# Performance work log

Measured on AMD Instinct MI355X. Metric: run time of the kernel, lower is better.

The kernel has to match this reference:

```python
import jax, jax.numpy as jnp
import numpy as np

B, H, F, Z, T = 8192, 256, 128, 64, 43
STEPS = T - 3


def setup_inputs() -> dict:
    key = jax.random.key(0)
    ks = jax.random.split(key, 24)
    def nrm(k, shape, s=0.05):
        return (jax.random.normal(k, shape) * s).astype(jnp.float32)
    inp = {}
    inp["h_i"] = nrm(ks[0], (B, H), 1.0)                      # encoder context state
    t = jax.random.uniform(ks[1], (B, T)) * T                  # event timestamps, sorted
    inp["input_t"] = jnp.sort(t, axis=1).astype(jnp.float32)
    inp["eps_inf"] = jax.random.normal(ks[2], (STEPS, B, Z), dtype=jnp.float32)
    inp["eps_prior"] = jax.random.normal(ks[3], (STEPS, B, Z), dtype=jnp.float32)
    in_dim = Z + H + F
    inp["Wx"] = nrm(ks[4], (in_dim, 4 * H))
    inp["Wh"] = nrm(ks[5], (H, 4 * H))
    inp["b_lstm"] = jnp.zeros((4 * H,), jnp.float32)
    dims = [(H, F), (F, F), (F, F), (2 * H + 2 * F, Z), (Z, Z), (Z, Z), (2 * H + F, Z), (Z, Z), (Z, Z)]
    for i, (di, do) in enumerate(dims, 1):
        inp[f"w{i}"] = nrm(ks[5 + i], (di, do))
        inp[f"b{i}"] = jnp.zeros((do,), jnp.float32)
    inp["alpha"] = (jax.random.uniform(ks[20], (1, 1)) * 0.1).astype(jnp.float32)
    inp["beta"] = (jax.random.uniform(ks[21], (1, 1)) * 0.1).astype(jnp.float32)
    inp["mu0"] = (jax.random.uniform(ks[22], (1, 1)) * 0.1).astype(jnp.float32)
    return inp


def _forward(h_i, input_t, eps_inf, eps_prior, Wx, Wh, b_lstm,
             w1, b1, w2, b2, w3, b3, w4, b4, w5, b5, w6, b6, w7, b7, w8, b8, w9, b9,
             alpha, beta, mu0):
    batch = h_i.shape[0]
    idxs = jnp.arange(T)

    def dense(x, w, b):
        return jax.nn.relu(x @ w + b)

    def step(carry, xs):
        h, c, z_j, y_prev = carry
        e_i, e_p, j = xs
        # LSTM cell (Keras gate order i, f, c, o)
        x = jnp.concatenate([z_j, h_i, y_prev], axis=1)
        gates = x @ Wx + h @ Wh + b_lstm
        i_g, f_g, g_g, o_g = jnp.split(gates, 4, axis=1)
        c_new = jax.nn.sigmoid(f_g) * c + jax.nn.sigmoid(i_g) * jnp.tanh(g_g)
        h_new = jax.nn.sigmoid(o_g) * jnp.tanh(c_new)
        # Hawkes intensity over events strictly before current_time_index = j+3
        t_idx = j + 3
        t_cur = jnp.take(input_t, t_idx, axis=1)[:, None]          # [B,1]
        mask = idxs < t_idx                                         # [T]
        diff = jnp.where(mask[None, :], input_t - t_cur, -jnp.inf)
        trig = jnp.sum(jnp.exp(diff), axis=1, keepdims=True) * beta[0, 0]
        intensity = mu0[0, 0] + alpha[0, 0] * trig                  # [B,1]
        # original code gates state[1] (the cell state slot) with the intensity
        c_gated = intensity * c_new
        y = dense(dense(dense(h_new, w1, b1), w2, b2), w3, b3)
        # inference network (s_j = ungated c_new, mirroring the TF code)
        inf_in = jnp.concatenate([h_i, c_new, y, y_prev], axis=1)
        hz = dense(inf_in, w4, b4)
        mean_j = dense(hz, w5, b5)
        lv_j = dense(hz, w6, b6)
        z_new = mean_j + e_i * jnp.sqrt(jnp.exp(lv_j))
        # prior network
        pri_in = jnp.concatenate([h_i, c_new, y_prev], axis=1)
        hzp = dense(pri_in, w7, b7)
        mean_p = dense(hzp, w8, b8)
        lv_p = dense(hzp, w9, b9)
        z_p = mean_p + e_p * jnp.sqrt(jnp.exp(lv_p))
        return (h_new, c_gated, z_new, y), (y, mean_j, lv_j, z_new, z_p)

    carry0 = (jnp.zeros((batch, H), h_i.dtype), jnp.zeros((batch, H), h_i.dtype),
              jnp.zeros((batch, Z), h_i.dtype), jnp.zeros((batch, F), h_i.dtype))
    xs = (eps_inf, eps_prior, jnp.arange(STEPS))
    _, (ys, means, lvs, zs, zps) = jax.lax.scan(step, carry0, xs)
    # [STEPS,B,*] -> [B,STEPS,*]
    tr = lambda a: jnp.transpose(a, (1, 0, 2))
    return tr(ys), tr(means), tr(lvs), tr(zs), tr(zps)


def reference(h_i, input_t, eps_inf, eps_prior, Wx, Wh, b_lstm,
              w1, b1, w2, b2, w3, b3, w4, b4, w5, b5, w6, b6, w7, b7, w8, b8, w9, b9,
              alpha, beta, mu0):
    return _forward(h_i, input_t, eps_inf, eps_prior, Wx, Wh, b_lstm,
                    w1, b1, w2, b2, w3, b3, w4, b4, w5, b5, w6, b6, w7, b7, w8, b8, w9, b9,
                    alpha, beta, mu0)
```

## Files before the change

### kernel.cpp

```cpp
#include <hip/hip_runtime.h>


#define BDIM  8192
#define HDIM  256
#define FDIM  128
#define ZDIM  64
#define TDIM  43
#define STEPS 40

typedef __attribute__((ext_vector_type(8))) __bf16 bf16x8;
typedef __attribute__((ext_vector_type(4))) float  f32x4;

#define ACT_STRIDE 3248
#define C_Z   0
#define C_Y0  64
#define C_Y1  192
#define C_H0  320
#define C_H1  576
#define C_C   832
#define C_T0  1088
#define C_T1  1216
#define C_HZ  1344
#define C_HZP 1408
#define C_B4  1472
#define C_B7  1536

#define PW_GS  0u
#define PW_GHI 458752u
#define PW_W1  720896u
#define PW_W2  753664u
#define PW_W3  770048u
#define PW_W4S 786432u
#define PW_W4H 819200u
#define PW_W5  835584u
#define PW_W6  839680u
#define PW_W7S 843776u
#define PW_W7H 868352u
#define PW_W8  884736u
#define PW_W9  888832u

__device__ __forceinline__ int act_off(int row, int col) {
  return row * ACT_STRIDE + ((row >> 3) << 4) + (col << 1);
}
__device__ __forceinline__ f32x4 mfma16(bf16x8 a, bf16x8 b, f32x4 c) {
  return __builtin_amdgcn_mfma_f32_16x16x32_bf16(a, b, c, 0, 0, 0);
}
__device__ __forceinline__ float sigm(float x) { return 1.f / (1.f + __expf(-x)); }
__device__ __forceinline__ float tanh_f(float x) {
  float t = __expf(-2.f * fabsf(x));
  float r = (1.f - t) / (1.f + t);
  return x < 0.f ? -r : r;
}
__device__ __forceinline__ void wg_barrier() {
  asm volatile("s_waitcnt lgkmcnt(0)" ::: "memory");
  __builtin_amdgcn_s_barrier();
  __builtin_amdgcn_sched_barrier(0);
}
__device__ __forceinline__ bf16x8 aread(const unsigned char* actb, int mt, int col,
                                        int lane) {
  return *(const bf16x8*)(actb + act_off(mt * 16 + (lane & 15), col + ((lane >> 4) << 3)));
}
__device__ __forceinline__ void st16(unsigned char* actb, int col, int mt, int rsub,
                                     f32x4 v, float bv) {
#pragma unroll
  for (int r = 0; r < 4; ++r)
    *(__bf16*)(actb + act_off(mt * 16 + rsub + r, col)) = (__bf16)fmaxf(v[r] + bv, 0.f);
}
__device__ __forceinline__ unsigned int pk2(float a, float b) {
  union { __bf16 h; unsigned short u; } x, y;
  x.h = (__bf16)a; y.h = (__bf16)b;
  return (unsigned int)x.u | ((unsigned int)y.u << 16);
}
__device__ __forceinline__ float upkf(unsigned int u, int hi) {
  union { unsigned int i; float f; } c;
  c.i = hi ? (u & 0xffff0000u) : (u << 16);
  return c.f;
}

struct PSeg { const float* p; int row0; int len; };

__global__ __launch_bounds__(256) void pack_w(PSeg s0, PSeg s1, PSeg s2,
                                              int K, int N, __bf16* __restrict__ dst) {
  int f = blockIdx.x * 256 + threadIdx.x;
  int KT = K >> 5;
  int total = KT * (N >> 4) * 64;
  if (f >= total) return;
  int lane = f & 63;
  int tile = f >> 6;
  int kt = tile % KT;
  int nt = tile / KT;
  int k0 = kt * 32 + ((lane >> 4) << 3);
  int n = (nt << 4) + (lane & 15);
  bf16x8 v;
#pragma unroll
  for (int j = 0; j < 8; ++j) {
    int k = k0 + j;
    const float* src;
    int r;
    if (k < s0.len) { src = s0.p; r = s0.row0 + k; }
    else if (k < s0.len + s1.len) { src = s1.p; r = s1.row0 + (k - s0.len); }
    else { src = s2.p; r = s2.row0 + (k - s0.len - s1.len); }
    v[j] = (__bf16)src[(size_t)r * N + n];
  }
  *(bf16x8*)(dst + (size_t)f * 8) = v;
}

struct Params {
  const float *h_i, *input_t, *eps_inf, *eps_prior;
  const float *b_lstm, *b1, *b2, *b3, *b4, *b5, *b6, *b7, *b8, *b9;
  const float *alpha, *beta, *mu0;
  const __bf16* wpack;
  float* out;
};

#define LDA(t, ktv)                                                         \
  do {                                                                      \
    _Pragma("unroll") for (int g = 0; g < 4; ++g) wb[t][g] =                \
        wgs[((size_t)(g * 16 + w) * 14 + (ktv)) * 64 + lane];               \
  } while (0)

__attribute__((amdgpu_waves_per_eu(4, 4)))
__global__ __launch_bounds__(1024) void decoder_main(Params p) {
  __shared__ __align__(16) unsigned char act[32 * ACT_STRIDE];
  __shared__ float fbuf[2048];
  __shared__ float inten[STEPS * 32];

  const int tid = threadIdx.x;
  const int w = tid >> 6;
  const int lane = tid & 63;
  const int ln16 = lane & 15;
  const int rsub = (lane >> 4) << 2;
  const int r0 = blockIdx.x * 32;

  for (int i = tid; i < (32 * ACT_STRIDE) / 4; i += 1024) ((unsigned int*)act)[i] = 0u;
  __syncthreads();
  for (int i = tid; i < 32 * 256; i += 1024) {
    int row = i >> 8, col = i & 255;
    *(__bf16*)(act + act_off(row, C_C + col)) =
        (__bf16)p.h_i[(size_t)(r0 + row) * HDIM + col];
  }
  {
    float ab = p.alpha[0] * p.beta[0], mu = p.mu0[0];
    for (int t = tid; t < 32 * STEPS; t += 1024) {
      int row = t & 31, j = t >> 5;
      const float* tp = p.input_t + (size_t)(r0 + row) * TDIM;
      float tc = tp[j + 3];
      float s = 0.f;
      for (int idx = 0; idx < j + 3; ++idx) s += __expf(tp[idx] - tc);
      inten[j * 32 + row] = mu + ab * s;
    }
  }
  __syncthreads();

  const __bf16* W = p.wpack;
  const bf16x8* wgs = (const bf16x8*)(W + PW_GS);
  const bf16x8* wghi = (const bf16x8*)(W + PW_GHI);
  const bf16x8* w1p = (const bf16x8*)(W + PW_W1);
  const bf16x8* w2p = (const bf16x8*)(W + PW_W2);
  const bf16x8* w3p = (const bf16x8*)(W + PW_W3);
  const bf16x8* w4s = (const bf16x8*)(W + PW_W4S);
  const bf16x8* w4h = (const bf16x8*)(W + PW_W4H);
  const bf16x8* w5p = (const bf16x8*)(W + PW_W5);
  const bf16x8* w6p = (const bf16x8*)(W + PW_W6);
  const bf16x8* w7s = (const bf16x8*)(W + PW_W7S);
  const bf16x8* w7h = (const bf16x8*)(W + PW_W7H);
  const bf16x8* w8p = (const bf16x8*)(W + PW_W8);
  const bf16x8* w9p = (const bf16x8*)(W + PW_W9);

  uint2 gbp[4][2];
  {
    f32x4 g[4][2] = {};
#pragma unroll
    for (int kt = 0; kt < 8; ++kt) {
      bf16x8 a0 = aread(act, 0, C_C + kt * 32, lane);
      bf16x8 a1 = aread(act, 1, C_C + kt * 32, lane);
#pragma unroll
      for (int gg = 0; gg < 4; ++gg) {
        bf16x8 b = wghi[((size_t)(gg * 16 + w) * 8 + kt) * 64 + lane];
        g[gg][0] = mfma16(a0, b, g[gg][0]);
        g[gg][1] = mfma16(a1, b, g[gg][1]);
      }
    }
#pragma unroll
    for (int gg = 0; gg < 4; ++gg) {
      float bv = p.b_lstm[gg * 256 + w * 16 + ln16];
#pragma unroll
      for (int mt = 0; mt < 2; ++mt) {
        gbp[gg][mt].x = pk2(g[gg][mt][0] + bv, g[gg][mt][1] + bv);
        gbp[gg][mt].y = pk2(g[gg][mt][2] + bv, g[gg][mt][3] + bv);
      }
    }
  }
  {
    int n = w & 3, mt = (w >> 2) & 1;
    const bf16x8* wp = (w < 8) ? w4h : w7h;
    const float* bb = (w < 8) ? p.b4 : p.b7;
    int cb = (w < 8) ? C_B4 : C_B7;
    f32x4 v = {};
#pragma unroll
    for (int kt = 0; kt < 8; ++kt)
      v = mfma16(aread(act, mt, C_C + kt * 32, lane),
                 wp[(size_t)(n * 8 + kt) * 64 + lane], v);
    float bv = bb[n * 16 + ln16];
#pragma unroll
    for (int r = 0; r < 4; ++r)
      *(__bf16*)(act + act_off(mt * 16 + rsub + r, cb + n * 16 + ln16)) =
          (__bf16)(v[r] + bv);
  }
  f32x4 c_st[2] = {};
  __syncthreads();

  float* outy = p.out;
  float* outm = p.out + (size_t)BDIM * STEPS * FDIM;
  float* outl = outm + (size_t)BDIM * STEPS * ZDIM;
  float* outz = outl + (size_t)BDIM * STEPS * ZDIM;
  float* outzp = outz + (size_t)BDIM * STEPS * ZDIM;

  bf16x8 wb[3][4];
  LDA(0, 0);
  LDA(1, 1);
  LDA(2, 2);

  for (int j = 0; j < STEPS; ++j) {
    const int yW = (j & 1) ? C_Y1 : C_Y0, yR = (j & 1) ? C_Y0 : C_Y1;
    const int hW = (j & 1) ? C_H1 : C_H0, hR = (j & 1) ? C_H0 : C_H1;

    {
      f32x4 acc[4][2] = {};
#pragma unroll
      for (int kt = 0; kt < 14; ++kt) {
        int col = (kt < 2) ? (C_Z + kt * 32)
                           : (kt < 6) ? (yR + (kt - 2) * 32) : (hR + (kt - 6) * 32);
        bf16x8 a0 = aread(act, 0, col, lane);
        bf16x8 a1 = aread(act, 1, col, lane);
        const int s = kt % 3;
#pragma unroll
        for (int g = 0; g < 4; ++g) {
          acc[g][0] = mfma16(a0, wb[s][g], acc[g][0]);
          acc[g][1] = mfma16(a1, wb[s][g], acc[g][1]);
        }
        if (kt + 3 < 14) LDA(s, kt + 3);
      }
#pragma unroll
      for (int mt = 0; mt < 2; ++mt) {
#pragma unroll
        for (int r = 0; r < 4; ++r) {
          int row = mt * 16 + rsub + r;
          unsigned int ui = (r < 2) ? gbp[0][mt].x : gbp[0][mt].y;
          unsigned int uf = (r < 2) ? gbp[1][mt].x : gbp[1][mt].y;
          unsigned int ug = (r < 2) ? gbp[2][mt].x : gbp[2][mt].y;
          unsigned int uo = (r < 2) ? gbp[3][mt].x : gbp[3][mt].y;
          float ig = sigm(acc[0][mt][r] + upkf(ui, r & 1));
          float fg = sigm(acc[1][mt][r] + upkf(uf, r & 1));
          float gg = tanh_f(acc[2][mt][r] + upkf(ug, r & 1));
          float og = sigm(acc[3][mt][r] + upkf(uo, r & 1));
          float cn = fg * c_st[mt][r] + ig * gg;
          float hn = og * tanh_f(cn);
          c_st[mt][r] = inten[j * 32 + row] * cn;
          *(__bf16*)(act + act_off(row, C_C + w * 16 + ln16)) = (__bf16)cn;
          *(__bf16*)(act + act_off(row, hW + w * 16 + ln16)) = (__bf16)hn;
        }
      }
    }
    wg_barrier();

    if (w < 8) {
      bf16x8 wf[8];
#pragma unroll
      for (int kt = 0; kt < 8; ++kt) wf[kt] = w1p[(size_t)(w * 8 + kt) * 64 + lane];
      f32x4 a0 = {}, a1 = {};
#pragma unroll
      for (int kt = 0; kt < 8; ++kt) {
        a0 = mfma16(aread(act, 0, hW + kt * 32, lane), wf[kt], a0);
        a1 = mfma16(aread(act, 1, hW + kt * 32, lane), wf[kt], a1);
      }
      float bv = p.b1[w * 16 + ln16];
      st16(act, C_T0 + w * 16 + ln16, 0, rsub, a0, bv);
      st16(act, C_T0 + w * 16 + ln16, 1, rsub, a1, bv);
    } else {
      int n = w & 3, mt = (w >> 2) & 1;
      bf16x8 wf[12];
#pragma unroll
      for (int kt = 0; kt < 12; ++kt) wf[kt] = w7s[(size_t)(n * 12 + kt) * 64 + lane];
      f32x4 v = {};
#pragma unroll
      for (int kt = 0; kt < 12; ++kt) {
        int col = (kt < 8) ? (C_C + kt * 32) : (yR + (kt - 8) * 32);
        v = mfma16(aread(act, mt, col, lane), wf[kt], v);
      }
#pragma unroll
      for (int r = 0; r < 4; ++r) {
        int row = mt * 16 + rsub + r;
        float s = v[r] + (float)*(const __bf16*)(act + act_off(row, C_B7 + n * 16 + ln16));
        *(__bf16*)(act + act_off(row, C_HZP + n * 16 + ln16)) = (__bf16)fmaxf(s, 0.f);
      }
    }
    wg_barrier();

    if (w < 8) {
      bf16x8 wf[4];
#pragma unroll
      for (int kt = 0; kt < 4; ++kt) wf[kt] = w2p[(size_t)(w * 4 + kt) * 64 + lane];
      f32x4 a0 = {}, a1 = {};
#pragma unroll
      for (int kt = 0; kt < 4; ++kt) {
        a0 = mfma16(aread(act, 0, C_T0 + kt * 32, lane), wf[kt], a0);
        a1 = mfma16(aread(act, 1, C_T0 + kt * 32, lane), wf[kt], a1);
      }
      float bv = p.b2[w * 16 + ln16];
      st16(act, C_T1 + w * 16 + ln16, 0, rsub, a0, bv);
      st16(act, C_T1 + w * 16 + ln16, 1, rsub, a1, bv);
    } else {
      int n = w & 3, mt = (w >> 2) & 1;
      float ep[4];
#pragma unroll
      for (int r = 0; r < 4; ++r)
        ep[r] = __builtin_nontemporal_load(
            p.eps_prior + ((size_t)j * BDIM + r0 + mt * 16 + rsub + r) * ZDIM +
            n * 16 + ln16);
      bf16x8 wm[2], wl[2];
#pragma unroll
      for (int kt = 0; kt < 2; ++kt) {
        wm[kt] = w8p[(size_t)(n * 2 + kt) * 64 + lane];
        wl[kt] = w9p[(size_t)(n * 2 + kt) * 64 + lane];
      }
      f32x4 vm = {}, vl = {};
#pragma unroll
      for (int kt = 0; kt < 2; ++kt) {
        bf16x8 a = aread(act, mt, C_HZP + kt * 32, lane);
        vm = mfma16(a, wm[kt], vm);
        vl = mfma16(a, wl[kt], vl);
      }
      float bm = p.b8[n * 16 + ln16], bl = p.b9[n * 16 + ln16];
#pragma unroll
      for (int r = 0; r < 4; ++r) {
        int row = mt * 16 + rsub + r, col = n * 16 + ln16;
        float mp = fmaxf(vm[r] + bm, 0.f), lp = fmaxf(vl[r] + bl, 0.f);
        float zp = mp + ep[r] * __expf(0.5f * lp);
        __builtin_nontemporal_store(
            zp, outzp + ((size_t)(r0 + row) * STEPS + j) * ZDIM + col);
      }
    }
    wg_barrier();

    if (w < 8) {
      bf16x8 wf[4];
#pragma unroll
      for (int kt = 0; kt < 4; ++kt) wf[kt] = w3p[(size_t)(w * 4 + kt) * 64 + lane];
      f32x4 a0 = {}, a1 = {};
#pragma unroll
      for (int kt = 0; kt < 4; ++kt) {
        a0 = mfma16(aread(act, 0, C_T1 + kt * 32, lane), wf[kt], a0);
        a1 = mfma16(aread(act, 1, C_T1 + kt * 32, lane), wf[kt], a1);
      }
      float bv = p.b3[w * 16 + ln16];
#pragma unroll
      for (int mt = 0; mt < 2; ++mt) {
        f32x4 vv = mt ? a1 : a0;
#pragma unroll
        for (int r = 0; r < 4; ++r) {
          int row = mt * 16 + rsub + r;
          float yv = fmaxf(vv[r] + bv, 0.f);
          *(__bf16*)(act + act_off(row, yW + w * 16 + ln16)) = (__bf16)yv;
          __builtin_nontemporal_store(
              yv, outy + ((size_t)(r0 + row) * STEPS + j) * FDIM + w * 16 + ln16);
        }
      }
    } else {
      int a = w - 8, n = a & 3, mt = a >> 2;
      bf16x8 wf[12];
#pragma unroll
      for (int kk = 0; kk < 12; ++kk) {
        int kt = (kk < 8) ? kk : (kk + 4);
        wf[kk] = w4s[(size_t)(n * 16 + kt) * 64 + lane];
      }
      f32x4 v = {};
#pragma unroll
      for (int kk = 0; kk < 12; ++kk) {
        int col = (kk < 8) ? (C_C + kk * 32) : (yR + (kk - 8) * 32);
        v = mfma16(aread(act, mt, col, lane), wf[kk], v);
      }
#pragma unroll
      for (int r = 0; r < 4; ++r)
        fbuf[(mt * 16 + rsub + r) * 64 + n * 16 + ln16] = v[r];
    }
    wg_barrier();

    LDA(0, 0);
    LDA(1, 1);
    LDA(2, 2);
    if (w < 8) {
      int n = w & 3, mt = w >> 2;
      bf16x8 wf[4];
#pragma unroll
      for (int kt = 8; kt < 12; ++kt) wf[kt - 8] = w4s[(size_t)(n * 16 + kt) * 64 + lane];
      f32x4 v = {};
#pragma unroll
      for (int kt = 8; kt < 12; ++kt)
        v = mfma16(aread(act, mt, yW + (kt - 8) * 32, lane), wf[kt - 8], v);
#pragma unroll
      for (int r = 0; r < 4; ++r) {
        int row = mt * 16 + rsub + r, cc = n * 16 + ln16;
        float s = v[r] + fbuf[row * 64 + cc] +
                  (float)*(const __bf16*)(act + act_off(row, C_B4 + cc));
        *(__bf16*)(act + act_off(row, C_HZ + cc)) = (__bf16)fmaxf(s, 0.f);
      }
    }
    wg_barrier();

    if (w < 8) {
      int n = w & 3, mt = w >> 2;
      float ei[4];
#pragma unroll
      for (int r = 0; r < 4; ++r)
        ei[r] = __builtin_nontemporal_load(
            p.eps_inf + ((size_t)j * BDIM + r0 + mt * 16 + rsub + r) * ZDIM +
            n * 16 + ln16);
      bf16x8 wm[2], wl[2];
#pragma unroll
      for (int kt = 0; kt < 2; ++kt) {
        wm[kt] = w5p[(size_t)(n * 2 + kt) * 64 + lane];
        wl[kt] = w6p[(size_t)(n * 2 + kt) * 64 + lane];
      }
      f32x4 vm = {}, vl = {};
#pragma unroll
      for (int kt = 0; kt < 2; ++kt) {
        bf16x8 a = aread(act, mt, C_HZ + kt * 32, lane);
        vm = mfma16(a, wm[kt], vm);
        vl = mfma16(a, wl[kt], vl);
      }
      float bm = p.b5[n * 16 + ln16], bl = p.b6[n * 16 + ln16];
#pragma unroll
      for (int r = 0; r < 4; ++r) {
        int row = mt * 16 + rsub + r, col = n * 16 + ln16;
        float m = fmaxf(vm[r] + bm, 0.f), l = fmaxf(vl[r] + bl, 0.f);
        float zn = m + ei[r] * __expf(0.5f * l);
        size_t ob = ((size_t)(r0 + row) * STEPS + j) * ZDIM + col;
        __builtin_nontemporal_store(m, outm + ob);
        __builtin_nontemporal_store(l, outl + ob);
        __builtin_nontemporal_store(zn, outz + ob);
        *(__bf16*)(act + act_off(row, C_Z + col)) = (__bf16)zn;
      }
    }
    wg_barrier();
  }
}

extern "C" void kernel_launch(void* const* d_in, const int* in_sizes, int n_in,
                              void* d_out, int out_size, void* d_ws, size_t ws_size,
                              hipStream_t stream) {
  const float* h_i = (const float*)d_in[0];
  const float* input_t = (const float*)d_in[1];
  const float* eps_inf = (const float*)d_in[2];
  const float* eps_prior = (const float*)d_in[3];
  const float* Wx = (const float*)d_in[4];
  const float* Wh = (const float*)d_in[5];
  const float* b_lstm = (const float*)d_in[6];
  const float* w1 = (const float*)d_in[7];  const float* b1 = (const float*)d_in[8];
  const float* w2 = (const float*)d_in[9];  const float* b2 = (const float*)d_in[10];
  const float* w3 = (const float*)d_in[11]; const float* b3 = (const float*)d_in[12];
  const float* w4 = (const float*)d_in[13]; const float* b4 = (const float*)d_in[14];
  const float* w5 = (const float*)d_in[15]; const float* b5 = (const float*)d_in[16];
  const float* w6 = (const float*)d_in[17]; const float* b6 = (const float*)d_in[18];
  const float* w7 = (const float*)d_in[19]; const float* b7 = (const float*)d_in[20];
  const float* w8 = (const float*)d_in[21]; const float* b8 = (const float*)d_in[22];
  const float* w9 = (const float*)d_in[23]; const float* b9 = (const float*)d_in[24];
  const float* alpha = (const float*)d_in[25];
  const float* beta = (const float*)d_in[26];
  const float* mu0 = (const float*)d_in[27];
  __bf16* ws = (__bf16*)d_ws;

  auto S = [](const float* ptr, int row0, int len) {
    PSeg s; s.p = ptr; s.row0 = row0; s.len = len; return s;
  };
  PSeg Zs; Zs.p = nullptr; Zs.row0 = 0; Zs.len = 0;
  auto L = [&](PSeg a, PSeg b, PSeg c, int K, int N, unsigned off) {
    int total = (K / 32) * (N / 16) * 64;
    pack_w<<<(total + 255) / 256, 256, 0, stream>>>(a, b, c, K, N, ws + off);
  };
  L(S(Wx, 0, 64), S(Wx, 320, 128), S(Wh, 0, 256), 448, 1024, PW_GS);
  L(S(Wx, 64, 256), Zs, Zs, 256, 1024, PW_GHI);
  L(S(w1, 0, 256), Zs, Zs, 256, 128, PW_W1);
  L(S(w2, 0, 128), Zs, Zs, 128, 128, PW_W2);
  L(S(w3, 0, 128), Zs, Zs, 128, 128, PW_W3);
  L(S(w4, 256, 512), Zs, Zs, 512, 64, PW_W4S);
  L(S(w4, 0, 256), Zs, Zs, 256, 64, PW_W4H);
  L(S(w5, 0, 64), Zs, Zs, 64, 64, PW_W5);
  L(S(w6, 0, 64), Zs, Zs, 64, 64, PW_W6);
  L(S(w7, 256, 384), Zs, Zs, 384, 64, PW_W7S);
  L(S(w7, 0, 256), Zs, Zs, 256, 64, PW_W7H);
  L(S(w8, 0, 64), Zs, Zs, 64, 64, PW_W8);
  L(S(w9, 0, 64), Zs, Zs, 64, 64, PW_W9);

  Params p;
  p.h_i = h_i; p.input_t = input_t; p.eps_inf = eps_inf; p.eps_prior = eps_prior;
  p.b_lstm = b_lstm; p.b1 = b1; p.b2 = b2; p.b3 = b3; p.b4 = b4; p.b5 = b5;
  p.b6 = b6; p.b7 = b7; p.b8 = b8; p.b9 = b9;
  p.alpha = alpha; p.beta = beta; p.mu0 = mu0;
  p.wpack = ws;
  p.out = (float*)d_out;

  decoder_main<<<256, 1024, 0, stream>>>(p);
}
```

Before: 2.403 ms.

## Interleave next-step LSTM gate GEMM chunks into the head stages with 512 threads

The LSTM gate GEMM now runs over the full input (z, h_i, y, h), split into 22 K-chunks. The chunks whose operands are already available are spread across the barrier-separated head stages (w1-w9), so each wave keeps its MFMA units busy between the small dependent GEMMs. The block shrinks to 8 waves that each own two gate column tiles and every head stage, which removes the idle split where half the waves sat out each stage. The cost is that the constant h_i gate contribution is recomputed every step instead of being precomputed once. Register pressure also rises from the larger accumulator set, and the old prefetch and fbuf path are dropped.

```diff
diff --git a/kernel.cpp b/kernel.cpp
--- a/kernel.cpp
+++ b/kernel.cpp
@@ -11,22 +11,20 @@
 typedef __attribute__((ext_vector_type(8))) __bf16 bf16x8;
 typedef __attribute__((ext_vector_type(4))) float  f32x4;
 
-#define ACT_STRIDE 3248
+#define ACT_STRIDE 3504
 #define C_Z   0
-#define C_Y0  64
-#define C_Y1  192
-#define C_H0  320
-#define C_H1  576
-#define C_C   832
-#define C_T0  1088
-#define C_T1  1216
-#define C_HZ  1344
-#define C_HZP 1408
-#define C_B4  1472
-#define C_B7  1536
+#define C_HI  64
+#define C_Y0  320
+#define C_Y1  448
+#define C_H0  576
+#define C_H1  832
+#define C_C   1088
+#define C_T0  1344
+#define C_T1  1472
+#define C_HZ  1600
+#define C_HZP 1664
 
 #define PW_GS  0u
-#define PW_GHI 458752u
 #define PW_W1  720896u
 #define PW_W2  753664u
 #define PW_W3  770048u
@@ -56,25 +54,15 @@
   __builtin_amdgcn_s_barrier();
   __builtin_amdgcn_sched_barrier(0);
 }
-__device__ __forceinline__ bf16x8 aread(const unsigned char* actb, int mt, int col,
-                                        int lane) {
-  return *(const bf16x8*)(actb + act_off(mt * 16 + (lane & 15), col + ((lane >> 4) << 3)));
-}
-__device__ __forceinline__ void st16(unsigned char* actb, int col, int mt, int rsub,
+__device__ __forceinline__ bf16x8 aread16(const unsigned char* a, int mt, int col,
+                                          int lane) {
+  return *(const bf16x8*)(a + act_off(mt * 16 + (lane & 15), col + ((lane >> 4) << 3)));
+}
+__device__ __forceinline__ void st16(unsigned char* a, int col, int mt, int rsub,
                                      f32x4 v, float bv) {
 #pragma unroll
   for (int r = 0; r < 4; ++r)
-    *(__bf16*)(actb + act_off(mt * 16 + rsub + r, col)) = (__bf16)fmaxf(v[r] + bv, 0.f);
-}
-__device__ __forceinline__ unsigned int pk2(float a, float b) {
-  union { __bf16 h; unsigned short u; } x, y;
-  x.h = (__bf16)a; y.h = (__bf16)b;
-  return (unsigned int)x.u | ((unsigned int)y.u << 16);
-}
-__device__ __forceinline__ float upkf(unsigned int u, int hi) {
-  union { unsigned int i; float f; } c;
-  c.i = hi ? (u & 0xffff0000u) : (u << 16);
-  return c.f;
+    *(__bf16*)(a + act_off(mt * 16 + rsub + r, col)) = (__bf16)fmaxf(v[r] + bv, 0.f);
 }
 
 struct PSeg { const float* p; int row0; int len; };
@@ -113,16 +101,9 @@
   float* out;
 };
 
-#define LDA(t, ktv)                                                         \
-  do {                                                                      \
-    _Pragma("unroll") for (int g = 0; g < 4; ++g) wb[t][g] =                \
-        wgs[((size_t)(g * 16 + w) * 14 + (ktv)) * 64 + lane];               \
-  } while (0)
-
-__attribute__((amdgpu_waves_per_eu(4, 4)))
-__global__ __launch_bounds__(1024) void decoder_main(Params p) {
+__global__ __launch_bounds__(512) __attribute__((amdgpu_waves_per_eu(2, 2)))
+void decoder_main(Params p) {
   __shared__ __align__(16) unsigned char act[32 * ACT_STRIDE];
-  __shared__ float fbuf[2048];
   __shared__ float inten[STEPS * 32];
 
   const int tid = threadIdx.x;
@@ -132,16 +113,16 @@
   const int rsub = (lane >> 4) << 2;
   const int r0 = blockIdx.x * 32;
 
-  for (int i = tid; i < (32 * ACT_STRIDE) / 4; i += 1024) ((unsigned int*)act)[i] = 0u;
+  for (int i = tid; i < (32 * ACT_STRIDE) / 4; i += 512) ((unsigned int*)act)[i] = 0u;
   __syncthreads();
-  for (int i = tid; i < 32 * 256; i += 1024) {
+  for (int i = tid; i < 32 * 256; i += 512) {
     int row = i >> 8, col = i & 255;
-    *(__bf16*)(act + act_off(row, C_C + col)) =
+    *(__bf16*)(act + act_off(row, C_HI + col)) =
         (__bf16)p.h_i[(size_t)(r0 + row) * HDIM + col];
   }
   {
     float ab = p.alpha[0] * p.beta[0], mu = p.mu0[0];
-    for (int t = tid; t < 32 * STEPS; t += 1024) {
+    for (int t = tid; t < 32 * STEPS; t += 512) {
       int row = t & 31, j = t >> 5;
       const float* tp = p.input_t + (size_t)(r0 + row) * TDIM;
       float tc = tp[j + 3];
@@ -154,7 +135,6 @@
 
   const __bf16* W = p.wpack;
   const bf16x8* wgs = (const bf16x8*)(W + PW_GS);
-  const bf16x8* wghi = (const bf16x8*)(W + PW_GHI);
   const bf16x8* w1p = (const bf16x8*)(W + PW_W1);
   const bf16x8* w2p = (const bf16x8*)(W + PW_W2);
   const bf16x8* w3p = (const bf16x8*)(W + PW_W3);
@@ -167,47 +147,34 @@
   const bf16x8* w8p = (const bf16x8*)(W + PW_W8);
   const bf16x8* w9p = (const bf16x8*)(W + PW_W9);
 
-  uint2 gbp[4][2];
+  const int n2 = w & 3, m2 = w >> 2;
+  f32x4 b4f = {}, b7f = {};
   {
-    f32x4 g[4][2] = {};
+    f32x4 v4 = {}, v7 = {};
 #pragma unroll
     for (int kt = 0; kt < 8; ++kt) {
-      bf16x8 a0 = aread(act, 0, C_C + kt * 32, lane);
-      bf16x8 a1 = aread(act, 1, C_C + kt * 32, lane);
-#pragma unroll
-      for (int gg = 0; gg < 4; ++gg) {
-        bf16x8 b = wghi[((size_t)(gg * 16 + w) * 8 + kt) * 64 + lane];
-        g[gg][0] = mfma16(a0, b, g[gg][0]);
-        g[gg][1] = mfma16(a1, b, g[gg][1]);
-      }
-    }
-#pragma unroll
-    for (int gg = 0; gg < 4; ++gg) {
-      float bv = p.b_lstm[gg * 256 + w * 16 + ln16];
-#pragma unroll
-      for (int mt = 0; mt < 2; ++mt) {
-        gbp[gg][mt].x = pk2(g[gg][mt][0] + bv, g[gg][mt][1] + bv);
-        gbp[gg][mt].y = pk2(g[gg][mt][2] + bv, g[gg][mt][3] + bv);
-      }
-    }
+      bf16x8 a = aread16(act, m2, C_HI + kt * 32, lane);
+      v4 = mfma16(a, w4h[(size_t)(n2 * 8 + kt) * 64 + lane], v4);
+      v7 = mfma16(a, w7h[(size_t)(n2 * 8 + kt) * 64 + lane], v7);
+    }
+    float b4v = p.b4[n2 * 16 + ln16], b7v = p.b7[n2 * 16 + ln16];
+#pragma unroll
+    for (int r = 0; r < 4; ++r) { b4f[r] = v4[r] + b4v; b7f[r] = v7[r] + b7v; }
   }
-  {
-    int n = w & 3, mt = (w >> 2) & 1;
-    const bf16x8* wp = (w < 8) ? w4h : w7h;
-    const float* bb = (w < 8) ? p.b4 : p.b7;
-    int cb = (w < 8) ? C_B4 : C_B7;
-    f32x4 v = {};
-#pragma unroll
-    for (int kt = 0; kt < 8; ++kt)
-      v = mfma16(aread(act, mt, C_C + kt * 32, lane),
-                 wp[(size_t)(n * 8 + kt) * 64 + lane], v);
-    float bv = bb[n * 16 + ln16];
-#pragma unroll
-    for (int r = 0; r < 4; ++r)
-      *(__bf16*)(act + act_off(mt * 16 + rsub + r, cb + n * 16 + ln16)) =
-          (__bf16)(v[r] + bv);
-  }
-  f32x4 c_st[2] = {};
+  float bg4[4][2];
+#pragma unroll
+  for (int g = 0; g < 4; ++g)
+#pragma unroll
+    for (int t = 0; t < 2; ++t)
+      bg4[g][t] = p.b_lstm[g * 256 + (w * 2 + t) * 16 + ln16];
+  const float bv1 = p.b1[w * 16 + ln16];
+  const float bv2 = p.b2[w * 16 + ln16];
+  const float bv3 = p.b3[w * 16 + ln16];
+  const float b5v = p.b5[n2 * 16 + ln16];
+  const float b6v = p.b6[n2 * 16 + ln16];
+  const float b8v = p.b8[n2 * 16 + ln16];
+  const float b9v = p.b9[n2 * 16 + ln16];
+  f32x4 c_st[2][2] = {};
   __syncthreads();
 
   float* outy = p.out;
@@ -216,224 +183,227 @@
   float* outz = outl + (size_t)BDIM * STEPS * ZDIM;
   float* outzp = outz + (size_t)BDIM * STEPS * ZDIM;
 
-  bf16x8 wb[3][4];
-  LDA(0, 0);
-  LDA(1, 1);
-  LDA(2, 2);
+  f32x4 acc[4][2][2] = {};
+
+#define GCHUNK(KT_, YCOL_, HCOL_)                                              \
+  do {                                                                         \
+    int col_ = ((KT_) < 2) ? (C_Z + (KT_)*32)                                  \
+               : ((KT_) < 10) ? (C_HI + ((KT_)-2) * 32)                        \
+               : ((KT_) < 14) ? ((YCOL_) + ((KT_)-10) * 32)                    \
+                              : ((HCOL_) + ((KT_)-14) * 32);                   \
+    bf16x8 a0_ = aread16(act, 0, col_, lane);                                  \
+    bf16x8 a1_ = aread16(act, 1, col_, lane);                                  \
+    _Pragma("unroll") for (int g_ = 0; g_ < 4; ++g_) {                         \
+      _Pragma("unroll") for (int t_ = 0; t_ < 2; ++t_) {                       \
+        bf16x8 b_ = wgs[((size_t)((g_ * 16 + w * 2 + t_) * 22 + (KT_))) * 64 + \
+                        lane];                                                 \
+        acc[g_][t_][0] = mfma16(a0_, b_, acc[g_][t_][0]);                      \
+        acc[g_][t_][1] = mfma16(a1_, b_, acc[g_][t_][1]);                      \
+      }                                                                        \
+    }                                                                          \
+  } while (0)
+
+#pragma unroll 2
+  for (int kt = 2; kt < 22; ++kt) GCHUNK(kt, C_Y1, C_H1);
 
   for (int j = 0; j < STEPS; ++j) {
     const int yW = (j & 1) ? C_Y1 : C_Y0, yR = (j & 1) ? C_Y0 : C_Y1;
-    const int hW = (j & 1) ? C_H1 : C_H0, hR = (j & 1) ? C_H0 : C_H1;
-
-    {
-      f32x4 acc[4][2] = {};
-#pragma unroll
-      for (int kt = 0; kt < 14; ++kt) {
-        int col = (kt < 2) ? (C_Z + kt * 32)
-                           : (kt < 6) ? (yR + (kt - 2) * 32) : (hR + (kt - 6) * 32);
-        bf16x8 a0 = aread(act, 0, col, lane);
-        bf16x8 a1 = aread(act, 1, col, lane);
-        const int s = kt % 3;
-#pragma unroll
-        for (int g = 0; g < 4; ++g) {
-          acc[g][0] = mfma16(a0, wb[s][g], acc[g][0]);
-          acc[g][1] = mfma16(a1, wb[s][g], acc[g][1]);
-        }
-        if (kt + 3 < 14) LDA(s, kt + 3);
-      }
-#pragma unroll
-      for (int mt = 0; mt < 2; ++mt) {
+    const int hW = (j & 1) ? C_H1 : C_H0;
+
+    GCHUNK(0, yW, hW);
+    GCHUNK(1, yW, hW);
+#pragma unroll
+    for (int t = 0; t < 2; ++t) {
+      int colc = (w * 2 + t) * 16 + ln16;
+#pragma unroll
+      for (int mt = 0; mt < 2; ++mt)
 #pragma unroll
         for (int r = 0; r < 4; ++r) {
           int row = mt * 16 + rsub + r;
-          unsigned int ui = (r < 2) ? gbp[0][mt].x : gbp[0][mt].y;
-          unsigned int uf = (r < 2) ? gbp[1][mt].x : gbp[1][mt].y;
-          unsigned int ug = (r < 2) ? gbp[2][mt].x : gbp[2][mt].y;
-          unsigned int uo = (r < 2) ? gbp[3][mt].x : gbp[3][mt].y;
-          float ig = sigm(acc[0][mt][r] + upkf(ui, r & 1));
-          float fg = sigm(acc[1][mt][r] + upkf(uf, r & 1));
-          float gg = tanh_f(acc[2][mt][r] + upkf(ug, r & 1));
-          float og = sigm(acc[3][mt][r] + upkf(uo, r & 1));
-          float cn = fg * c_st[mt][r] + ig * gg;
+          float ig = sigm(acc[0][t][mt][r] + bg4[0][t]);
+          float fg = sigm(acc[1][t][mt][r] + bg4[1][t]);
+          float gg = tanh_f(acc[2][t][mt][r] + bg4[2][t]);
+          float og = sigm(acc[3][t][mt][r] + bg4[3][t]);
+          float cn = fg * c_st[t][mt][r] + ig * gg;
           float hn = og * tanh_f(cn);
-          c_st[mt][r] = inten[j * 32 + row] * cn;
-          *(__bf16*)(act + act_off(row, C_C + w * 16 + ln16)) = (__bf16)cn;
-          *(__bf16*)(act + act_off(row, hW + w * 16 + ln16)) = (__bf16)hn;
+          c_st[t][mt][r] = inten[j * 32 + row] * cn;
+          *(__bf16*)(act + act_off(row, C_C + colc)) = (__bf16)cn;
+          *(__bf16*)(act + act_off(row, hW + colc)) = (__bf16)hn;
         }
-      }
-    }
-    wg_barrier();
-
-    if (w < 8) {
+    }
+#pragma unroll
+    for (int g = 0; g < 4; ++g)
+#pragma unroll
+      for (int t = 0; t < 2; ++t)
+#pragma unroll
+        for (int mt = 0; mt < 2; ++mt) acc[g][t][mt] = (f32x4){0.f, 0.f, 0.f, 0.f};
+    wg_barrier();
+
+    {
       bf16x8 wf[8];
 #pragma unroll
       for (int kt = 0; kt < 8; ++kt) wf[kt] = w1p[(size_t)(w * 8 + kt) * 64 + lane];
       f32x4 a0 = {}, a1 = {};
 #pragma unroll
       for (int kt = 0; kt < 8; ++kt) {
-        a0 = mfma16(aread(act, 0, hW + kt * 32, lane), wf[kt], a0);
-        a1 = mfma16(aread(act, 1, hW + kt * 32, lane), wf[kt], a1);
-      }
-      float bv = p.b1[w * 16 + ln16];
-      st16(act, C_T0 + w * 16 + ln16, 0, rsub, a0, bv);
-      st16(act, C_T0 + w * 16 + ln16, 1, rsub, a1, bv);
-    } else {
-      int n = w & 3, mt = (w >> 2) & 1;
+        a0 = mfma16(aread16(act, 0, hW + kt * 32, lane), wf[kt], a0);
+        a1 = mfma16(aread16(act, 1, hW + kt * 32, lane), wf[kt], a1);
+      }
+      st16(act, C_T0 + w * 16 + ln16, 0, rsub, a0, bv1);
+      st16(act, C_T0 + w * 16 + ln16, 1, rsub, a1, bv1);
+    }
+    {
       bf16x8 wf[12];
 #pragma unroll
-      for (int kt = 0; kt < 12; ++kt) wf[kt] = w7s[(size_t)(n * 12 + kt) * 64 + lane];
+      for (int kt = 0; kt < 12; ++kt) wf[kt] = w7s[(size_t)(n2 * 12 + kt) * 64 + lane];
       f32x4 v = {};
 #pragma unroll
       for (int kt = 0; kt < 12; ++kt) {
         int col = (kt < 8) ? (C_C + kt * 32) : (yR + (kt - 8) * 32);
-        v = mfma16(aread(act, mt, col, lane), wf[kt], v);
-      }
-#pragma unroll
-      for (int r = 0; r < 4; ++r) {
-        int row = mt * 16 + rsub + r;
-        float s = v[r] + (float)*(const __bf16*)(act + act_off(row, C_B7 + n * 16 + ln16));
-        *(__bf16*)(act + act_off(row, C_HZP + n * 16 + ln16)) = (__bf16)fmaxf(s, 0.f);
-      }
-    }
-    wg_barrier();
-
-    if (w < 8) {
+        v = mfma16(aread16(act, m2, col, lane), wf[kt], v);
+      }
+#pragma unroll
+      for (int r = 0; r < 4; ++r)
+        *(__bf16*)(act + act_off(m2 * 16 + rsub + r, C_HZP + n2 * 16 + ln16)) =
+            (__bf16)fmaxf(v[r] + b7f[r], 0.f);
+    }
+    GCHUNK(14, yW, hW);
+    GCHUNK(15, yW, hW);
+    GCHUNK(2, yW, hW);
+    GCHUNK(3, yW, hW);
+    wg_barrier();
+
+    {
       bf16x8 wf[4];
 #pragma unroll
       for (int kt = 0; kt < 4; ++kt) wf[kt] = w2p[(size_t)(w * 4 + kt) * 64 + lane];
       f32x4 a0 = {}, a1 = {};
 #pragma unroll
       for (int kt = 0; kt < 4; ++kt) {
-        a0 = mfma16(aread(act, 0, C_T0 + kt * 32, lane), wf[kt], a0);
-        a1 = mfma16(aread(act, 1, C_T0 + kt * 32, lane), wf[kt], a1);
-      }
-      float bv = p.b2[w * 16 + ln16];
-      st16(act, C_T1 + w * 16 + ln16, 0, rsub, a0, bv);
-      st16(act, C_T1 + w * 16 + ln16, 1, rsub, a1, bv);
-    } else {
-      int n = w & 3, mt = (w >> 2) & 1;
+        a0 = mfma16(aread16(act, 0, C_T0 + kt * 32, lane), wf[kt], a0);
+        a1 = mfma16(aread16(act, 1, C_T0 + kt * 32, lane), wf[kt], a1);
+      }
+      st16(act, C_T1 + w * 16 + ln16, 0, rsub, a0, bv2);
+      st16(act, C_T1 + w * 16 + ln16, 1, rsub, a1, bv2);
+    }
+    {
+      bf16x8 wm[2], wl[2];
       float ep[4];
 #pragma unroll
+      for (int kt = 0; kt < 2; ++kt) {
+        wm[kt] = w8p[(size_t)(n2 * 2 + kt) * 64 + lane];
+        wl[kt] = w9p[(size_t)(n2 * 2 + kt) * 64 + lane];
+      }
+#pragma unroll
       for (int r = 0; r < 4; ++r)
-        ep[r] = __builtin_nontemporal_load(
-            p.eps_prior + ((size_t)j * BDIM + r0 + mt * 16 + rsub + r) * ZDIM +
-            n * 16 + ln16);
-      bf16x8 wm[2], wl[2];
+        ep[r] = p.eps_prior[((size_t)j * BDIM + r0 + m2 * 16 + rsub + r) * ZDIM +
+                            n2 * 16 + ln16];
+      f32x4 vm = {}, vl = {};
 #pragma unroll
       for (int kt = 0; kt < 2; ++kt) {
-        wm[kt] = w8p[(size_t)(n * 2 + kt) * 64 + lane];
-        wl[kt] = w9p[(size_t)(n * 2 + kt) * 64 + lane];
-      }
-      f32x4 vm = {}, vl = {};
-#pragma unroll
-      for (int kt = 0; kt < 2; ++kt) {
-        bf16x8 a = aread(act, mt, C_HZP + kt * 32, lane);
+        bf16x8 a = aread16(act, m2, C_HZP + kt * 32, lane);
         vm = mfma16(a, wm[kt], vm);
         vl = mfma16(a, wl[kt], vl);
       }
-      float bm = p.b8[n * 16 + ln16], bl = p.b9[n * 16 + ln16];
 #pragma unroll
       for (int r = 0; r < 4; ++r) {
-        int row = mt * 16 + rsub + r, col = n * 16 + ln16;
-        float mp = fmaxf(vm[r] + bm, 0.f), lp = fmaxf(vl[r] + bl, 0.f);
+        float mp = fmaxf(vm[r] + b8v, 0.f), lp = fmaxf(vl[r] + b9v, 0.f);
         float zp = mp + ep[r] * __expf(0.5f * lp);
         __builtin_nontemporal_store(
-            zp, outzp + ((size_t)(r0 + row) * STEPS + j) * ZDIM + col);
-      }
-    }
-    wg_barrier();
-
-    if (w < 8) {
+            zp, outzp + ((size_t)(r0 + m2 * 16 + rsub + r) * STEPS + j) * ZDIM +
+                    n2 * 16 + ln16);
+      }
+    }
+    GCHUNK(16, yW, hW);
+    GCHUNK(17, yW, hW);
+    GCHUNK(4, yW, hW);
+    GCHUNK(5, yW, hW);
+    wg_barrier();
+
+    {
       bf16x8 wf[4];
 #pragma unroll
       for (int kt = 0; kt < 4; ++kt) wf[kt] = w3p[(size_t)(w * 4 + kt) * 64 + lane];
       f32x4 a0 = {}, a1 = {};
 #pragma unroll
       for (int kt = 0; kt < 4; ++kt) {
-        a0 = mfma16(aread(act, 0, C_T1 + kt * 32, lane), wf[kt], a0);
-        a1 = mfma16(aread(act, 1, C_T1 + kt * 32, lane), wf[kt], a1);
-      }
-      float bv = p.b3[w * 16 + ln16];
+        a0 = mfma16(aread16(act, 0, C_T1 + kt * 32, lane), wf[kt], a0);
+        a1 = mfma16(aread16(act, 1, C_T1 + kt * 32, lane), wf[kt], a1);
+      }
 #pragma unroll
       for (int mt = 0; mt < 2; ++mt) {
         f32x4 vv = mt ? a1 : a0;
 #pragma unroll
         for (int r = 0; r < 4; ++r) {
           int row = mt * 16 + rsub + r;
-          float yv = fmaxf(vv[r] + bv, 0.f);
+          float yv = fmaxf(vv[r] + bv3, 0.f);
           *(__bf16*)(act + act_off(row, yW + w * 16 + ln16)) = (__bf16)yv;
           __builtin_nontemporal_store(
               yv, outy + ((size_t)(r0 + row) * STEPS + j) * FDIM + w * 16 + ln16);
         }
       }
-    } else {
-      int a = w - 8, n = a & 3, mt = a >> 2;
-      bf16x8 wf[12];
-#pragma unroll
-      for (int kk = 0; kk < 12; ++kk) {
-        int kt = (kk < 8) ? kk : (kk + 4);
-        wf[kk] = w4s[(size_t)(n * 16 + kt) * 64 + lane];
-      }
+    }
+    GCHUNK(18, yW, hW);
+    GCHUNK(19, yW, hW);
+    GCHUNK(6, yW, hW);
+    GCHUNK(7, yW, hW);
+    wg_barrier();
+
+    {
       f32x4 v = {};
-#pragma unroll
-      for (int kk = 0; kk < 12; ++kk) {
-        int col = (kk < 8) ? (C_C + kk * 32) : (yR + (kk - 8) * 32);
-        v = mfma16(aread(act, mt, col, lane), wf[kk], v);
+      {
+        bf16x8 wf[8];
+#pragma unroll
+        for (int kt = 0; kt < 8; ++kt) wf[kt] = w4s[(size_t)(n2 * 16 + kt) * 64 + lane];
+#pragma unroll
+        for (int kt = 0; kt < 8; ++kt)
+          v = mfma16(aread16(act, m2, C_C + kt * 32, lane), wf[kt], v);
+      }
+      {
+        bf16x8 wf[8];
+#pragma unroll
+        for (int kt = 8; kt < 16; ++kt)
+          wf[kt - 8] = w4s[(size_t)(n2 * 16 + kt) * 64 + lane];
+#pragma unroll
+        for (int kt = 8; kt < 16; ++kt) {
+          int col = (kt < 12) ? (yW + (kt - 8) * 32) : (yR + (kt - 12) * 32);
+          v = mfma16(aread16(act, m2, col, lane), wf[kt - 8], v);
+        }
       }
 #pragma unroll
       for (int r = 0; r < 4; ++r)
-        fbuf[(mt * 16 + rsub + r) * 64 + n * 16 + ln16] = v[r];
-    }
-    wg_barrier();
-
-    LDA(0, 0);
-    LDA(1, 1);
-    LDA(2, 2);
-    if (w < 8) {
-      int n = w & 3, mt = w >> 2;
-      bf16x8 wf[4];
-#pragma unroll
-      for (int kt = 8; kt < 12; ++kt) wf[kt - 8] = w4s[(size_t)(n * 16 + kt) * 64 + lane];
-      f32x4 v = {};
-#pragma unroll
-      for (int kt = 8; kt < 12; ++kt)
-        v = mfma16(aread(act, mt, yW + (kt - 8) * 32, lane), wf[kt - 8], v);
-#pragma unroll
-      for (int r = 0; r < 4; ++r) {
-        int row = mt * 16 + rsub + r, cc = n * 16 + ln16;
-        float s = v[r] + fbuf[row * 64 + cc] +
-                  (float)*(const __bf16*)(act + act_off(row, C_B4 + cc));
-        *(__bf16*)(act + act_off(row, C_HZ + cc)) = (__bf16)fmaxf(s, 0.f);
-      }
-    }
-    wg_barrier();
-
-    if (w < 8) {
-      int n = w & 3, mt = w >> 2;
+        *(__bf16*)(act + act_off(m2 * 16 + rsub + r, C_HZ + n2 * 16 + ln16)) =
+            (__bf16)fmaxf(v[r] + b4f[r], 0.f);
+    }
+    GCHUNK(20, yW, hW);
+    GCHUNK(21, yW, hW);
+    GCHUNK(8, yW, hW);
+    GCHUNK(9, yW, hW);
+    wg_barrier();
+
+    {
+      bf16x8 wm[2], wl[2];
       float ei[4];
 #pragma unroll
+      for (int kt = 0; kt < 2; ++kt) {
+        wm[kt] = w5p[(size_t)(n2 * 2 + kt) * 64 + lane];
+        wl[kt] = w6p[(size_t)(n2 * 2 + kt) * 64 + lane];
+      }
+#pragma unroll
       for (int r = 0; r < 4; ++r)
-        ei[r] = __builtin_nontemporal_load(
-            p.eps_inf + ((size_t)j * BDIM + r0 + mt * 16 + rsub + r) * ZDIM +
-            n * 16 + ln16);
-      bf16x8 wm[2], wl[2];
+        ei[r] = p.eps_inf[((size_t)j * BDIM + r0 + m2 * 16 + rsub + r) * ZDIM +
+                          n2 * 16 + ln16];
+      f32x4 vm = {}, vl = {};
 #pragma unroll
       for (int kt = 0; kt < 2; ++kt) {
-        wm[kt] = w5p[(size_t)(n * 2 + kt) * 64 + lane];
-        wl[kt] = w6p[(size_t)(n * 2 + kt) * 64 + lane];
-      }
-      f32x4 vm = {}, vl = {};
-#pragma unroll
-      for (int kt = 0; kt < 2; ++kt) {
-        bf16x8 a = aread(act, mt, C_HZ + kt * 32, lane);
+        bf16x8 a = aread16(act, m2, C_HZ + kt * 32, lane);
         vm = mfma16(a, wm[kt], vm);
         vl = mfma16(a, wl[kt], vl);
       }
-      float bm = p.b5[n * 16 + ln16], bl = p.b6[n * 16 + ln16];
 #pragma unroll
       for (int r = 0; r < 4; ++r) {
-        int row = mt * 16 + rsub + r, col = n * 16 + ln16;
-        float m = fmaxf(vm[r] + bm, 0.f), l = fmaxf(vl[r] + bl, 0.f);
+        int row = m2 * 16 + rsub + r, col = n2 * 16 + ln16;
+        float m = fmaxf(vm[r] + b5v, 0.f), l = fmaxf(vl[r] + b6v, 0.f);
         float zn = m + ei[r] * __expf(0.5f * l);
         size_t ob = ((size_t)(r0 + row) * STEPS + j) * ZDIM + col;
         __builtin_nontemporal_store(m, outm + ob);
@@ -442,8 +412,13 @@
         *(__bf16*)(act + act_off(row, C_Z + col)) = (__bf16)zn;
       }
     }
+    GCHUNK(10, yW, hW);
+    GCHUNK(11, yW, hW);
+    GCHUNK(12, yW, hW);
+    GCHUNK(13, yW, hW);
     wg_barrier();
   }
+#undef GCHUNK
 }
 
 extern "C" void kernel_launch(void* const* d_in, const int* in_sizes, int n_in,
@@ -478,8 +453,7 @@
     int total = (K / 32) * (N / 16) * 64;
     pack_w<<<(total + 255) / 256, 256, 0, stream>>>(a, b, c, K, N, ws + off);
   };
-  L(S(Wx, 0, 64), S(Wx, 320, 128), S(Wh, 0, 256), 448, 1024, PW_GS);
-  L(S(Wx, 64, 256), Zs, Zs, 256, 1024, PW_GHI);
+  L(S(Wx, 0, 448), S(Wh, 0, 256), Zs, 704, 1024, PW_GS);
   L(S(w1, 0, 256), Zs, Zs, 256, 128, PW_W1);
   L(S(w2, 0, 128), Zs, Zs, 128, 128, PW_W2);
   L(S(w3, 0, 128), Zs, Zs, 128, 128, PW_W3);
@@ -500,5 +474,5 @@
   p.wpack = ws;
   p.out = (float*)d_out;
 
-  decoder_main<<<256, 1024, 0, stream>>>(p);
-}
+  decoder_main<<<256, 512, 0, stream>>>(p);
+}
```

Result: slower. 3.836 ms (+59.7%).
